# Kernel optimization log

Hardware: AMD Instinct MI355X
Metric: run time of the kernel (lower is better)

The kernel has to match this reference:

```python
import jax, jax.numpy as jnp
import numpy as np

B, N, M, D = 8, 512, 64, 128
H = 64  # mlp_hidden_dim


def setup_inputs() -> dict:
    key = jax.random.key(0)
    ks = jax.random.split(key, 10)
    op_emb = jax.random.normal(ks[0], (B, N, D), dtype=jnp.float32)
    machine_emb = jax.random.normal(ks[1], (B, M, D), dtype=jnp.float32)
    edge_emb = jax.random.normal(ks[2], (B, N, M, D), dtype=jnp.float32)
    action_mask = jax.random.randint(ks[3], (B, N, M), 0, 2) > 0
    s1 = 1.0 / np.sqrt(3 * D)
    s2 = 1.0 / np.sqrt(H)
    W1 = jax.random.uniform(ks[4], (3 * D, H), jnp.float32, -s1, s1)
    b1 = jax.random.uniform(ks[5], (H,), jnp.float32, -s1, s1)
    W2 = jax.random.uniform(ks[6], (H, H), jnp.float32, -s2, s2)
    b2 = jax.random.uniform(ks[7], (H,), jnp.float32, -s2, s2)
    W3 = jax.random.uniform(ks[8], (H, 1), jnp.float32, -s2, s2)
    b3 = jax.random.uniform(ks[9], (1,), jnp.float32, -s2, s2)
    return {"op_emb": op_emb, "machine_emb": machine_emb, "edge_emb": edge_emb,
            "action_mask": action_mask,
            "W1": W1, "b1": b1, "W2": W2, "b2": b2, "W3": W3, "b3": b3}


def reference(op_emb, machine_emb, edge_emb, action_mask, W1, b1, W2, b2, W3, b3):
    # Split first linear over the three concat chunks to avoid materializing
    # the (B,N,M,3D) concat tensor (same math as cat -> Linear).
    Wo, Wm, We = W1[:D], W1[D:2 * D], W1[2 * D:]
    h = (jnp.einsum('bnd,dh->bnh', op_emb, Wo)[:, :, None, :]
         + jnp.einsum('bmd,dh->bmh', machine_emb, Wm)[:, None, :, :]
         + jnp.einsum('bnmd,dh->bnmh', edge_emb, We) + b1)  # (B,N,M,H)
    h = jax.nn.relu(h)
    h = jax.nn.relu(h @ W2 + b2)
    scores = (h @ W3 + b3)[..., 0]  # (B,N,M)
    scores = jnp.where(action_mask, scores, -jnp.inf)
    return jax.nn.log_softmax(scores.reshape(B, N * M), axis=-1)
```

## Files before the change

kernel.cpp:

```cpp
#include <hip/hip_runtime.h>
#include <math.h>

#define Bb 8
#define Nn 512
#define Mm 64
#define Dd 128
#define Hh 64
#define Gg 4
#define NEG_BIG (-1.0e30f)

typedef __bf16 bf16x8 __attribute__((ext_vector_type(8)));
typedef float  f32x4  __attribute__((ext_vector_type(4)));

#define WS_WEB   0u
#define WS_W2B   16384u
#define WS_CWS   24576u
#define WS_AOP   155648u
#define WS_SCORE 1204224u
#define WS_PART  2252800u
#define WS_CC    2256896u

__global__ __launch_bounds__(256) void wprep_kernel(
    const float* __restrict__ W1, const float* __restrict__ W2, char* __restrict__ ws)
{
    __bf16* WeB = (__bf16*)(ws + WS_WEB);
    __bf16* W2B = (__bf16*)(ws + WS_W2B);
    int idx = blockIdx.x * 256 + threadIdx.x;
    if (idx < 8192) {
        int fid = idx >> 9, rem = idx & 511;
        int lane = rem >> 3, j = rem & 7;
        int t = fid >> 2, ks = fid & 3;
        int q = lane >> 4, ln = lane & 15;
        int d = ks * 32 + q * 8 + j;
        int h = t * 16 + ln;
        WeB[idx] = (__bf16)W1[(size_t)(2 * Dd + d) * Hh + h];
    } else if (idx < 12288) {
        int i2 = idx - 8192;
        int fid = i2 >> 9, rem = i2 & 511;
        int lane = rem >> 3, j = rem & 7;
        int t = fid >> 1, ks = fid & 1;
        int q = lane >> 4, ln = lane & 15;
        int k = ks * 32 + q * 8 + j;
        int h = t * 16 + ln;
        W2B[i2] = (__bf16)W2[(size_t)k * Hh + h];
    }
}

__global__ __launch_bounds__(64) void proj_kernel(
    const float* __restrict__ op_emb, const float* __restrict__ machine_emb,
    const float* __restrict__ W1, const float* __restrict__ b1, char* __restrict__ ws)
{
    float* Cws = (float*)(ws + WS_CWS);
    float* Aop = (float*)(ws + WS_AOP);
    const int bid = blockIdx.x;
    const int h = threadIdx.x;
    if (bid < Bb * Mm) {
        const float* mg = machine_emb + (size_t)bid * Dd;
        const float* Wm = W1 + (size_t)Dd * Hh;
        float acc = b1[h];
#pragma unroll 8
        for (int d = 0; d < Dd; ++d) acc = fmaf(mg[d], Wm[d * Hh + h], acc);
        Cws[(size_t)bid * Hh + h] = acc;
    } else {
        const int bn = bid - Bb * Mm;
        const float* og = op_emb + (size_t)bn * Dd;
        float acc = 0.f;
#pragma unroll 8
        for (int d = 0; d < Dd; ++d) acc = fmaf(og[d], W1[d * Hh + h], acc);
        Aop[(size_t)bn * Hh + h] = acc;
    }
}

__global__ __launch_bounds__(256, 3) void main_kernel(
    const float* __restrict__ edge_emb, const int* __restrict__ mask,
    const float* __restrict__ b2, const float* __restrict__ W3,
    const float* __restrict__ b3, char* __restrict__ ws)
{
    __shared__ __bf16 sWeB[8192];
    __shared__ __bf16 sW2B[4096];
    __shared__ float  sCws[Mm * Hh];
    __shared__ __bf16 sH1[Mm * 72];
    __shared__ float  sAop[Gg * Hh];
    __shared__ int    sMask[Gg * Mm];

    float* scores = (float*)(ws + WS_SCORE);

    const int tid  = threadIdx.x;
    const int lane = tid & 63;
    const int w    = tid >> 6;
    const int q    = lane >> 4;
    const int ln   = lane & 15;
    const int bn0  = blockIdx.x * Gg;
    const int b    = bn0 >> 9;
    const int mrow = w * 16 + ln;

    {
        const float4* s1 = (const float4*)(ws + WS_WEB);
        float4* d1 = (float4*)sWeB;
        for (int i = tid; i < 1024; i += 256) d1[i] = s1[i];
        const float4* s2 = (const float4*)(ws + WS_W2B);
        float4* d2 = (float4*)sW2B;
        for (int i = tid; i < 512; i += 256) d2[i] = s2[i];
        const float4* s3 = (const float4*)(ws + WS_CWS) + (size_t)b * (Mm * Hh / 4);
        float4* d3 = (float4*)sCws;
        for (int i = tid; i < 1024; i += 256) d3[i] = s3[i];
        sAop[tid] = ((const float*)(ws + WS_AOP))[(size_t)bn0 * Hh + tid];
        sMask[tid] = mask[(size_t)bn0 * Mm + tid];
    }

    float b2v[4], w3v[4];
#pragma unroll
    for (int t = 0; t < 4; ++t) { b2v[t] = b2[t * 16 + ln]; w3v[t] = W3[t * 16 + ln]; }
    const float bias3 = b3[0];

    const float* Eg0 = edge_emb + (size_t)bn0 * (Mm * Dd) + mrow * Dd + q * 8;
    float4 raw[8];
#pragma unroll
    for (int ks = 0; ks < 4; ++ks) {
        raw[2 * ks]     = *(const float4*)&Eg0[ks * 32];
        raw[2 * ks + 1] = *(const float4*)&Eg0[ks * 32 + 4];
    }

    __syncthreads();

#pragma unroll
    for (int g = 0; g < Gg; ++g) {
        const int bn = bn0 + g;

        bf16x8 af[4];
#pragma unroll
        for (int ks = 0; ks < 4; ++ks) {
            float4 lo = raw[2 * ks], hi = raw[2 * ks + 1];
            bf16x8 a;
            a[0] = (__bf16)lo.x; a[1] = (__bf16)lo.y; a[2] = (__bf16)lo.z; a[3] = (__bf16)lo.w;
            a[4] = (__bf16)hi.x; a[5] = (__bf16)hi.y; a[6] = (__bf16)hi.z; a[7] = (__bf16)hi.w;
            af[ks] = a;
        }
        if (g + 1 < Gg) {
            const float* Eg = edge_emb + (size_t)(bn + 1) * (Mm * Dd) + mrow * Dd + q * 8;
#pragma unroll
            for (int ks = 0; ks < 4; ++ks) {
                raw[2 * ks]     = *(const float4*)&Eg[ks * 32];
                raw[2 * ks + 1] = *(const float4*)&Eg[ks * 32 + 4];
            }
        }

        f32x4 acc[4];
#pragma unroll
        for (int t = 0; t < 4; ++t) {
            float av = sAop[g * Hh + t * 16 + ln];
#pragma unroll
            for (int r = 0; r < 4; ++r)
                acc[t][r] = av + sCws[(w * 16 + q * 4 + r) * Hh + t * 16 + ln];
        }

#pragma unroll
        for (int t = 0; t < 4; ++t)
#pragma unroll
            for (int ks = 0; ks < 4; ++ks) {
                bf16x8 bfr = *(const bf16x8*)&sWeB[((t * 4 + ks) * 64 + lane) * 8];
                acc[t] = __builtin_amdgcn_mfma_f32_16x16x32_bf16(af[ks], bfr, acc[t], 0, 0, 0);
            }

#pragma unroll
        for (int t = 0; t < 4; ++t)
#pragma unroll
            for (int r = 0; r < 4; ++r)
                sH1[(w * 16 + q * 4 + r) * 72 + t * 16 + ln] =
                    (__bf16)fmaxf(acc[t][r], 0.f);

        bf16x8 a2[2];
#pragma unroll
        for (int ks = 0; ks < 2; ++ks)
            a2[ks] = *(const bf16x8*)&sH1[(w * 16 + ln) * 72 + ks * 32 + q * 8];
        f32x4 c2[4];
#pragma unroll
        for (int t = 0; t < 4; ++t) c2[t] = (f32x4){0.f, 0.f, 0.f, 0.f};
#pragma unroll
        for (int t = 0; t < 4; ++t)
#pragma unroll
            for (int ks = 0; ks < 2; ++ks) {
                bf16x8 bfr = *(const bf16x8*)&sW2B[((t * 2 + ks) * 64 + lane) * 8];
                c2[t] = __builtin_amdgcn_mfma_f32_16x16x32_bf16(a2[ks], bfr, c2[t], 0, 0, 0);
            }

        float p[4] = {0.f, 0.f, 0.f, 0.f};
#pragma unroll
        for (int t = 0; t < 4; ++t)
#pragma unroll
            for (int r = 0; r < 4; ++r)
                p[r] += fmaxf(c2[t][r] + b2v[t], 0.f) * w3v[t];
#pragma unroll
        for (int r = 0; r < 4; ++r) {
            p[r] += __shfl_xor(p[r], 1, 64);
            p[r] += __shfl_xor(p[r], 2, 64);
            p[r] += __shfl_xor(p[r], 4, 64);
            p[r] += __shfl_xor(p[r], 8, 64);
        }
        if (ln == 0) {
            int m0 = w * 16 + q * 4;
            float4 o;
            o.x = sMask[g * Mm + m0 + 0] ? (p[0] + bias3) : NEG_BIG;
            o.y = sMask[g * Mm + m0 + 1] ? (p[1] + bias3) : NEG_BIG;
            o.z = sMask[g * Mm + m0 + 2] ? (p[2] + bias3) : NEG_BIG;
            o.w = sMask[g * Mm + m0 + 3] ? (p[3] + bias3) : NEG_BIG;
            *(float4*)&scores[(size_t)bn * Mm + m0] = o;
        }
    }
}

__global__ __launch_bounds__(256) void lsm_part_kernel(char* __restrict__ ws)
{
    const float* s = (const float*)(ws + WS_SCORE);
    float* part = (float*)(ws + WS_PART);
    __shared__ float sm[4], ss[4];
    const int c = blockIdx.x;
    const int tid = threadIdx.x;
    const int lane = tid & 63, wv = tid >> 6;

    float2 v = *(const float2*)&s[(size_t)c * 512 + tid * 2];
    float m = fmaxf(v.x, v.y);
#pragma unroll
    for (int off = 1; off < 64; off <<= 1) m = fmaxf(m, __shfl_xor(m, off, 64));
    if (lane == 0) sm[wv] = m;
    __syncthreads();
    float gm = fmaxf(fmaxf(sm[0], sm[1]), fmaxf(sm[2], sm[3]));

    float e = expf(v.x - gm) + expf(v.y - gm);
#pragma unroll
    for (int off = 1; off < 64; off <<= 1) e += __shfl_xor(e, off, 64);
    if (lane == 0) ss[wv] = e;
    __syncthreads();
    if (tid == 0) {
        float2 o; o.x = gm; o.y = ss[0] + ss[1] + ss[2] + ss[3];
        *(float2*)&part[c * 2] = o;
    }
}

__global__ __launch_bounds__(64) void lsm_comb_kernel(char* __restrict__ ws)
{
    const float* part = (const float*)(ws + WS_PART);
    float* cc = (float*)(ws + WS_CC);
    const int b = blockIdx.x, t = threadIdx.x;
    float2 p = *(const float2*)&part[(b * 64 + t) * 2];
    float gm = p.x;
#pragma unroll
    for (int off = 1; off < 64; off <<= 1) gm = fmaxf(gm, __shfl_xor(gm, off, 64));
    float l = p.y * expf(p.x - gm);
#pragma unroll
    for (int off = 1; off < 64; off <<= 1) l += __shfl_xor(l, off, 64);
    if (t == 0) cc[b] = gm + logf(l);
}

__global__ __launch_bounds__(256) void lsm_apply_kernel(
    const char* __restrict__ ws, float* __restrict__ out)
{
    const float4* s4 = (const float4*)(ws + WS_SCORE);
    const float* cc = (const float*)(ws + WS_CC);
    const int i = blockIdx.x * 256 + threadIdx.x;
    const float c = cc[i >> 13];
    float4 v = s4[i];
    v.x -= c; v.y -= c; v.z -= c; v.w -= c;
    ((float4*)out)[i] = v;
}

extern "C" void kernel_launch(void* const* d_in, const int* in_sizes, int n_in,
                              void* d_out, int out_size, void* d_ws, size_t ws_size,
                              hipStream_t stream)
{
    const float* op_emb      = (const float*)d_in[0];
    const float* machine_emb = (const float*)d_in[1];
    const float* edge_emb    = (const float*)d_in[2];
    const int*   mask        = (const int*)  d_in[3];
    const float* W1 = (const float*)d_in[4];
    const float* b1 = (const float*)d_in[5];
    const float* W2 = (const float*)d_in[6];
    const float* b2 = (const float*)d_in[7];
    const float* W3 = (const float*)d_in[8];
    const float* b3 = (const float*)d_in[9];
    char* ws = (char*)d_ws;

    wprep_kernel<<<48, 256, 0, stream>>>(W1, W2, ws);
    proj_kernel<<<Bb * Mm + Bb * Nn, 64, 0, stream>>>(op_emb, machine_emb, W1, b1, ws);
    main_kernel<<<(Bb * Nn) / Gg, 256, 0, stream>>>(edge_emb, mask, b2, W3, b3, ws);
    lsm_part_kernel<<<512, 256, 0, stream>>>(ws);
    lsm_comb_kernel<<<Bb, 64, 0, stream>>>(ws);
    lsm_apply_kernel<<<256, 256, 0, stream>>>(ws, (float*)d_out);
}
```

Before: 238.5 us.

## Merge prep kernels, fold LSE combine into apply, drop main kernel LDS staging

The weight-prep and projection kernels are merged into one launch, and the log-sum-exp combine step is folded into the apply kernel, so two fewer launches and fewer dependency boundaries are needed. The main kernel stops staging weights, the machine projection, the op projection and the mask in shared memory. It reads the MFMA B fragments directly from global memory, keeps the C and op values in registers, and prefetches the next row's op projection and mask along with the edge tile. The occupancy hint is raised from 3 to 4 blocks per CU. In exchange, every wave now reloads the weight fragments from global or L2 memory on each iteration, and register pressure goes up.

```diff
diff --git a/kernel.cpp b/kernel.cpp
--- a/kernel.cpp
+++ b/kernel.cpp
@@ -18,42 +18,40 @@
 #define WS_AOP   155648u
 #define WS_SCORE 1204224u
 #define WS_PART  2252800u
-#define WS_CC    2256896u
-
-__global__ __launch_bounds__(256) void wprep_kernel(
-    const float* __restrict__ W1, const float* __restrict__ W2, char* __restrict__ ws)
-{
-    __bf16* WeB = (__bf16*)(ws + WS_WEB);
-    __bf16* W2B = (__bf16*)(ws + WS_W2B);
-    int idx = blockIdx.x * 256 + threadIdx.x;
-    if (idx < 8192) {
-        int fid = idx >> 9, rem = idx & 511;
-        int lane = rem >> 3, j = rem & 7;
-        int t = fid >> 2, ks = fid & 3;
-        int q = lane >> 4, ln = lane & 15;
-        int d = ks * 32 + q * 8 + j;
-        int h = t * 16 + ln;
-        WeB[idx] = (__bf16)W1[(size_t)(2 * Dd + d) * Hh + h];
-    } else if (idx < 12288) {
-        int i2 = idx - 8192;
-        int fid = i2 >> 9, rem = i2 & 511;
-        int lane = rem >> 3, j = rem & 7;
-        int t = fid >> 1, ks = fid & 1;
-        int q = lane >> 4, ln = lane & 15;
-        int k = ks * 32 + q * 8 + j;
-        int h = t * 16 + ln;
-        W2B[i2] = (__bf16)W2[(size_t)k * Hh + h];
-    }
-}
-
-__global__ __launch_bounds__(64) void proj_kernel(
+
+__global__ __launch_bounds__(256) void prep_kernel(
+    const float* __restrict__ W1, const float* __restrict__ W2,
     const float* __restrict__ op_emb, const float* __restrict__ machine_emb,
-    const float* __restrict__ W1, const float* __restrict__ b1, char* __restrict__ ws)
-{
+    const float* __restrict__ b1, char* __restrict__ ws)
+{
+    if (blockIdx.x < 48) {
+        __bf16* WeB = (__bf16*)(ws + WS_WEB);
+        __bf16* W2B = (__bf16*)(ws + WS_W2B);
+        int idx = blockIdx.x * 256 + threadIdx.x;
+        if (idx < 8192) {
+            int fid = idx >> 9, rem = idx & 511;
+            int lane = rem >> 3, j = rem & 7;
+            int t = fid >> 2, ks = fid & 3;
+            int q = lane >> 4, ln = lane & 15;
+            int d = ks * 32 + q * 8 + j;
+            int h = t * 16 + ln;
+            WeB[idx] = (__bf16)W1[(size_t)(2 * Dd + d) * Hh + h];
+        } else {
+            int i2 = idx - 8192;
+            int fid = i2 >> 9, rem = i2 & 511;
+            int lane = rem >> 3, j = rem & 7;
+            int t = fid >> 1, ks = fid & 1;
+            int q = lane >> 4, ln = lane & 15;
+            int k = ks * 32 + q * 8 + j;
+            int h = t * 16 + ln;
+            W2B[i2] = (__bf16)W2[(size_t)k * Hh + h];
+        }
+        return;
+    }
     float* Cws = (float*)(ws + WS_CWS);
     float* Aop = (float*)(ws + WS_AOP);
-    const int bid = blockIdx.x;
-    const int h = threadIdx.x;
+    const int bid = (blockIdx.x - 48) * 4 + (threadIdx.x >> 6);
+    const int h = threadIdx.x & 63;
     if (bid < Bb * Mm) {
         const float* mg = machine_emb + (size_t)bid * Dd;
         const float* Wm = W1 + (size_t)Dd * Hh;
@@ -71,19 +69,18 @@
     }
 }
 
-__global__ __launch_bounds__(256, 3) void main_kernel(
+__global__ __launch_bounds__(256, 4) void main_kernel(
     const float* __restrict__ edge_emb, const int* __restrict__ mask,
     const float* __restrict__ b2, const float* __restrict__ W3,
     const float* __restrict__ b3, char* __restrict__ ws)
 {
-    __shared__ __bf16 sWeB[8192];
-    __shared__ __bf16 sW2B[4096];
-    __shared__ float  sCws[Mm * Hh];
     __shared__ __bf16 sH1[Mm * 72];
-    __shared__ float  sAop[Gg * Hh];
-    __shared__ int    sMask[Gg * Mm];
-
-    float* scores = (float*)(ws + WS_SCORE);
+
+    const __bf16* WeB = (const __bf16*)(ws + WS_WEB);
+    const __bf16* W2B = (const __bf16*)(ws + WS_W2B);
+    const float*  Cws = (const float*)(ws + WS_CWS);
+    const float*  Aop = (const float*)(ws + WS_AOP);
+    float* scores     = (float*)(ws + WS_SCORE);
 
     const int tid  = threadIdx.x;
     const int lane = tid & 63;
@@ -94,34 +91,29 @@
     const int b    = bn0 >> 9;
     const int mrow = w * 16 + ln;
 
-    {
-        const float4* s1 = (const float4*)(ws + WS_WEB);
-        float4* d1 = (float4*)sWeB;
-        for (int i = tid; i < 1024; i += 256) d1[i] = s1[i];
-        const float4* s2 = (const float4*)(ws + WS_W2B);
-        float4* d2 = (float4*)sW2B;
-        for (int i = tid; i < 512; i += 256) d2[i] = s2[i];
-        const float4* s3 = (const float4*)(ws + WS_CWS) + (size_t)b * (Mm * Hh / 4);
-        float4* d3 = (float4*)sCws;
-        for (int i = tid; i < 1024; i += 256) d3[i] = s3[i];
-        sAop[tid] = ((const float*)(ws + WS_AOP))[(size_t)bn0 * Hh + tid];
-        sMask[tid] = mask[(size_t)bn0 * Mm + tid];
-    }
-
+    float cv[16];
+#pragma unroll
+    for (int t = 0; t < 4; ++t)
+#pragma unroll
+        for (int r = 0; r < 4; ++r)
+            cv[t * 4 + r] = Cws[((size_t)b * Mm + w * 16 + q * 4 + r) * Hh + t * 16 + ln];
     float b2v[4], w3v[4];
 #pragma unroll
     for (int t = 0; t < 4; ++t) { b2v[t] = b2[t * 16 + ln]; w3v[t] = W3[t * 16 + ln]; }
     const float bias3 = b3[0];
 
-    const float* Eg0 = edge_emb + (size_t)bn0 * (Mm * Dd) + mrow * Dd + q * 8;
-    float4 raw[8];
-#pragma unroll
-    for (int ks = 0; ks < 4; ++ks) {
-        raw[2 * ks]     = *(const float4*)&Eg0[ks * 32];
-        raw[2 * ks + 1] = *(const float4*)&Eg0[ks * 32 + 4];
-    }
-
-    __syncthreads();
+    float4 raw[8]; float aopv[4]; int4 mk = {0, 0, 0, 0};
+    {
+        const float* Eg = edge_emb + (size_t)bn0 * (Mm * Dd) + mrow * Dd + q * 8;
+#pragma unroll
+        for (int ks = 0; ks < 4; ++ks) {
+            raw[2 * ks]     = *(const float4*)&Eg[ks * 32];
+            raw[2 * ks + 1] = *(const float4*)&Eg[ks * 32 + 4];
+        }
+#pragma unroll
+        for (int t = 0; t < 4; ++t) aopv[t] = Aop[(size_t)bn0 * Hh + t * 16 + ln];
+        if (ln == 0) mk = *(const int4*)&mask[(size_t)bn0 * Mm + w * 16 + q * 4];
+    }
 
 #pragma unroll
     for (int g = 0; g < Gg; ++g) {
@@ -136,6 +128,8 @@
             a[4] = (__bf16)hi.x; a[5] = (__bf16)hi.y; a[6] = (__bf16)hi.z; a[7] = (__bf16)hi.w;
             af[ks] = a;
         }
+        float naop[4] = {};
+        int4  nmk = {0, 0, 0, 0};
         if (g + 1 < Gg) {
             const float* Eg = edge_emb + (size_t)(bn + 1) * (Mm * Dd) + mrow * Dd + q * 8;
 #pragma unroll
@@ -143,22 +137,23 @@
                 raw[2 * ks]     = *(const float4*)&Eg[ks * 32];
                 raw[2 * ks + 1] = *(const float4*)&Eg[ks * 32 + 4];
             }
+#pragma unroll
+            for (int t = 0; t < 4; ++t) naop[t] = Aop[(size_t)(bn + 1) * Hh + t * 16 + ln];
+            if (ln == 0) nmk = *(const int4*)&mask[(size_t)(bn + 1) * Mm + w * 16 + q * 4];
         }
 
         f32x4 acc[4];
 #pragma unroll
-        for (int t = 0; t < 4; ++t) {
-            float av = sAop[g * Hh + t * 16 + ln];
+        for (int t = 0; t < 4; ++t)
 #pragma unroll
             for (int r = 0; r < 4; ++r)
-                acc[t][r] = av + sCws[(w * 16 + q * 4 + r) * Hh + t * 16 + ln];
-        }
+                acc[t][r] = aopv[t] + cv[t * 4 + r];
 
 #pragma unroll
         for (int t = 0; t < 4; ++t)
 #pragma unroll
             for (int ks = 0; ks < 4; ++ks) {
-                bf16x8 bfr = *(const bf16x8*)&sWeB[((t * 4 + ks) * 64 + lane) * 8];
+                bf16x8 bfr = *(const bf16x8*)&WeB[((t * 4 + ks) * 64 + lane) * 8];
                 acc[t] = __builtin_amdgcn_mfma_f32_16x16x32_bf16(af[ks], bfr, acc[t], 0, 0, 0);
             }
 
@@ -180,7 +175,7 @@
         for (int t = 0; t < 4; ++t)
 #pragma unroll
             for (int ks = 0; ks < 2; ++ks) {
-                bf16x8 bfr = *(const bf16x8*)&sW2B[((t * 2 + ks) * 64 + lane) * 8];
+                bf16x8 bfr = *(const bf16x8*)&W2B[((t * 2 + ks) * 64 + lane) * 8];
                 c2[t] = __builtin_amdgcn_mfma_f32_16x16x32_bf16(a2[ks], bfr, c2[t], 0, 0, 0);
             }
 
@@ -198,14 +193,16 @@
             p[r] += __shfl_xor(p[r], 8, 64);
         }
         if (ln == 0) {
-            int m0 = w * 16 + q * 4;
             float4 o;
-            o.x = sMask[g * Mm + m0 + 0] ? (p[0] + bias3) : NEG_BIG;
-            o.y = sMask[g * Mm + m0 + 1] ? (p[1] + bias3) : NEG_BIG;
-            o.z = sMask[g * Mm + m0 + 2] ? (p[2] + bias3) : NEG_BIG;
-            o.w = sMask[g * Mm + m0 + 3] ? (p[3] + bias3) : NEG_BIG;
-            *(float4*)&scores[(size_t)bn * Mm + m0] = o;
-        }
+            o.x = mk.x ? (p[0] + bias3) : NEG_BIG;
+            o.y = mk.y ? (p[1] + bias3) : NEG_BIG;
+            o.z = mk.z ? (p[2] + bias3) : NEG_BIG;
+            o.w = mk.w ? (p[3] + bias3) : NEG_BIG;
+            *(float4*)&scores[(size_t)bn * Mm + w * 16 + q * 4] = o;
+        }
+#pragma unroll
+        for (int t = 0; t < 4; ++t) aopv[t] = naop[t];
+        mk = nmk;
     }
 }
 
@@ -237,28 +234,27 @@
     }
 }
 
-__global__ __launch_bounds__(64) void lsm_comb_kernel(char* __restrict__ ws)
-{
-    const float* part = (const float*)(ws + WS_PART);
-    float* cc = (float*)(ws + WS_CC);
-    const int b = blockIdx.x, t = threadIdx.x;
-    float2 p = *(const float2*)&part[(b * 64 + t) * 2];
-    float gm = p.x;
-#pragma unroll
-    for (int off = 1; off < 64; off <<= 1) gm = fmaxf(gm, __shfl_xor(gm, off, 64));
-    float l = p.y * expf(p.x - gm);
-#pragma unroll
-    for (int off = 1; off < 64; off <<= 1) l += __shfl_xor(l, off, 64);
-    if (t == 0) cc[b] = gm + logf(l);
-}
-
 __global__ __launch_bounds__(256) void lsm_apply_kernel(
     const char* __restrict__ ws, float* __restrict__ out)
 {
     const float4* s4 = (const float4*)(ws + WS_SCORE);
-    const float* cc = (const float*)(ws + WS_CC);
-    const int i = blockIdx.x * 256 + threadIdx.x;
-    const float c = cc[i >> 13];
+    const float* part = (const float*)(ws + WS_PART);
+    __shared__ float sCC;
+    const int tid = threadIdx.x;
+    const int b = blockIdx.x >> 5;
+    if (tid < 64) {
+        float2 p = *(const float2*)&part[(b * 64 + tid) * 2];
+        float gm = p.x;
+#pragma unroll
+        for (int off = 1; off < 64; off <<= 1) gm = fmaxf(gm, __shfl_xor(gm, off, 64));
+        float l = p.y * expf(p.x - gm);
+#pragma unroll
+        for (int off = 1; off < 64; off <<= 1) l += __shfl_xor(l, off, 64);
+        if (tid == 0) sCC = gm + logf(l);
+    }
+    __syncthreads();
+    const float c = sCC;
+    const int i = blockIdx.x * 256 + tid;
     float4 v = s4[i];
     v.x -= c; v.y -= c; v.z -= c; v.w -= c;
     ((float4*)out)[i] = v;
@@ -280,10 +276,8 @@
     const float* b3 = (const float*)d_in[9];
     char* ws = (char*)d_ws;
 
-    wprep_kernel<<<48, 256, 0, stream>>>(W1, W2, ws);
-    proj_kernel<<<Bb * Mm + Bb * Nn, 64, 0, stream>>>(op_emb, machine_emb, W1, b1, ws);
+    prep_kernel<<<48 + 1152, 256, 0, stream>>>(W1, W2, op_emb, machine_emb, b1, ws);
     main_kernel<<<(Bb * Nn) / Gg, 256, 0, stream>>>(edge_emb, mask, b2, W3, b3, ws);
     lsm_part_kernel<<<512, 256, 0, stream>>>(ws);
-    lsm_comb_kernel<<<Bb, 64, 0, stream>>>(ws);
     lsm_apply_kernel<<<256, 256, 0, stream>>>(ws, (float*)d_out);
 }
```

Measured after the change: 267.3 us. 1.12x slower.
